# Kernel optimization log

Measured on AMD Instinct MI355X. Metric: run time of the kernel, lower is better.

Reference implementation:

```python
import math
import jax, jax.numpy as jnp
import numpy as np

L, B, E, NDIM = 4096, 4, 1024, 16


def setup_inputs() -> dict:
    key = jax.random.key(0)
    ks = jax.random.split(key, 6)
    x = jax.random.normal(ks[0], (L, B, E), dtype=jnp.float32)
    alpha = jax.random.normal(ks[1], (2 * E, NDIM, 1), dtype=jnp.float32) * 0.2
    delta = jax.random.normal(ks[2], (2 * E, NDIM, 1), dtype=jnp.float32) * 0.2
    # beta init: N(0, 0.02) + alternating +-1 along ndim
    val = np.ones((NDIM, 1), dtype=np.float32)
    val[1::2] = -1.0
    beta = jax.random.normal(ks[3], (2 * E, NDIM, 1), dtype=jnp.float32) * 0.02 + jnp.asarray(val)
    gamma = jax.random.normal(ks[4], (2 * E, NDIM), dtype=jnp.float32)
    omega = jax.random.normal(ks[5], (E,), dtype=jnp.float32)
    return {"x": x, "alpha": alpha, "delta": delta, "beta": beta, "gamma": gamma, "omega": omega}


def reference(x, alpha, delta, beta, gamma, omega):
    seq_len, bsz, embed_dim = x.shape
    ndim = alpha.shape[1]
    scale = math.sqrt(1.0 / ndim)

    residual = x * omega  # (L, B, E)
    xc = jnp.transpose(x, (1, 2, 0))  # (B, E, L)

    a = jax.nn.sigmoid(alpha)
    d = jax.nn.sigmoid(delta)
    q = 1.0 - a * d          # (2E, ndim, 1)
    p = a * beta             # (2E, ndim, 1)

    t = jnp.arange(seq_len, dtype=x.dtype)          # (L,)
    vander = t[None, None, :] * jnp.log(q)          # (2E, ndim, L)
    kernel = p * jnp.exp(vander)                    # (2E, ndim, L)
    k = jnp.einsum('dnl,dn->dl', kernel, gamma * scale)  # (2E, L)

    fft_len = 2 * seq_len  # seq_len + kernel_size (truncation=None)
    k1, k2 = k[:embed_dim], k[embed_dim:]
    # bidirectional + shift: causal part padded right, flipped anti-causal padded left
    kb = jnp.pad(k1, ((0, 0), (0, seq_len))) + jnp.pad(k2[:, ::-1], ((0, 0), (seq_len, 0)))  # (E, 2L)

    k_f = jnp.fft.rfft(kb, n=fft_len)   # (E, L+1) complex
    x_f = jnp.fft.rfft(xc, n=fft_len)   # (B, E, L+1) complex
    out = jnp.fft.irfft(x_f * k_f, n=fft_len)[..., :seq_len]  # (B, E, L)
    out = out.astype(x.dtype)

    return jax.nn.silu(jnp.transpose(out, (2, 0, 1)) + residual)  # (L, B, E)
```

## Files before the change

kernel.cpp:

```cpp
#include <hip/hip_runtime.h>
#include <hip/hip_fp16.h>
#include <math.h>

#define L_  4096
#define B_  4
#define E_  1024
#define ND  16
#define BE  (B_*E_)
#define COLS (BE*ND)

#define OFF_Q   0
#define OFF_W   (2*E_*ND)
#define OFF_QC  (2*2*E_*ND)
#define OFF_FS  (3*2*E_*ND)

__device__ __forceinline__ float sigm(float x){ return 1.0f/(1.0f+__expf(-x)); }

__global__ void k_params(const float* __restrict__ al,
                         const float* __restrict__ de,
                         const float* __restrict__ be,
                         const float* __restrict__ ga,
                         float* __restrict__ ws, int lg){
    int i = blockIdx.x*256 + threadIdx.x;
    float a = sigm(al[i]);
    float d = sigm(de[i]);
    float q = 1.0f - a*d;
    float w = a*be[i]*ga[i]*0.25f;
    float qc = q;
    for(int k=0;k<lg;k++) qc *= qc;
    ws[OFF_Q+i]=q; ws[OFF_W+i]=w; ws[OFF_QC+i]=qc;
}

template<int CK>
__global__ __launch_bounds__(256) void k_summ_t(const float* __restrict__ x,
                                                float* __restrict__ ws){
    const int bid = blockIdx.x;
    const int c  = bid >> 4;
    const int b  = (bid >> 2) & 3;
    const int eg = bid & 3;
    const int e  = eg*256 + threadIdx.x;
    const float* Q = ws + OFF_Q;
    float qf[ND], qb[ND], F[ND], G[ND], pw[ND];
    #pragma unroll
    for(int n=0;n<ND;n++){
        qf[n]=Q[e*ND+n]; qb[n]=Q[(E_+e)*ND+n];
        F[n]=0.f; G[n]=0.f; pw[n]=1.f;
    }
    const float* xp = x + (size_t)(c*CK)*BE + b*E_ + e;
    #pragma unroll 4
    for(int i=0;i<CK;i++){
        float xv = xp[(size_t)i*BE];
        #pragma unroll
        for(int n=0;n<ND;n++){
            F[n]=fmaf(qf[n],F[n],xv);
            G[n]=fmaf(pw[n],xv,G[n]);
            pw[n]*=qb[n];
        }
    }
    const int col = (b*E_+e)*ND;
    float* Fp = ws + OFF_FS + (size_t)c*COLS + col;
    float* Gp = ws + OFF_FS + (size_t)(L_/CK)*COLS + (size_t)c*COLS + col;
    #pragma unroll
    for(int n=0;n<ND;n++){ Fp[n]=F[n]; Gp[n]=G[n]; }
}

template<int CK, int CW>
__global__ __launch_bounds__(256) void k_out2_t(const float* __restrict__ x,
                                                const float* __restrict__ om,
                                                const float* __restrict__ ws,
                                                float* __restrict__ out){
    constexpr int NC = L_/CK;
    __shared__ __half part[CK*256];
    const int tid = threadIdx.x;
    const int bid = blockIdx.x;
    const int c  = bid >> 4;
    const int b  = (bid >> 2) & 3;
    const int eg = bid & 3;
    const int e  = eg*256 + tid;
    const float* Q = ws + OFF_Q;
    const float* W = ws + OFF_W;
    const float omg = om[e];
    const int col = (b*E_+e)*ND;
    const float* xp = x + (size_t)(c*CK)*BE + b*E_ + e;
    const float* FS = ws + OFF_FS;
    const float* GR = ws + OFF_FS + (size_t)NC*COLS;

    {
        float st[ND];
        {
            float pw[ND], qcf[ND];
            #pragma unroll
            for(int n=0;n<ND;n++){ st[n]=0.f; pw[n]=1.f; qcf[n]=ws[OFF_QC+e*ND+n]; }
            int jm = (c < CW) ? c : CW;
            for(int j=1;j<=jm;j++){
                const float4* Fp = (const float4*)(FS + (size_t)(c-j)*COLS + col);
                #pragma unroll
                for(int v=0;v<4;v++){
                    float4 f = Fp[v];
                    st[4*v+0]=fmaf(pw[4*v+0],f.x,st[4*v+0]);
                    st[4*v+1]=fmaf(pw[4*v+1],f.y,st[4*v+1]);
                    st[4*v+2]=fmaf(pw[4*v+2],f.z,st[4*v+2]);
                    st[4*v+3]=fmaf(pw[4*v+3],f.w,st[4*v+3]);
                }
                #pragma unroll
                for(int n=0;n<ND;n++) pw[n]*=qcf[n];
            }
        }
        float q1[ND], w1[ND];
        #pragma unroll
        for(int n=0;n<ND;n++){ q1[n]=Q[e*ND+n]; w1[n]=W[e*ND+n]; }
        #pragma unroll 4
        for(int i=0;i<CK;i++){
            float xv = xp[(size_t)i*BE];
            float acc = xv*omg;
            #pragma unroll
            for(int n=0;n<ND;n++){ st[n]=fmaf(q1[n],st[n],xv); acc=fmaf(w1[n],st[n],acc); }
            part[i*256+tid] = __float2half_rn(acc);
        }
    }

    {
        float rt[ND];
        {
            float pw[ND], qcb[ND];
            #pragma unroll
            for(int n=0;n<ND;n++){ rt[n]=0.f; pw[n]=1.f; qcb[n]=ws[OFF_QC+(E_+e)*ND+n]; }
            int jm = NC-1-c; if(jm > CW) jm = CW;
            for(int j=1;j<=jm;j++){
                const float4* Gp = (const float4*)(GR + (size_t)(c+j)*COLS + col);
                #pragma unroll
                for(int v=0;v<4;v++){
                    float4 g = Gp[v];
                    rt[4*v+0]=fmaf(pw[4*v+0],g.x,rt[4*v+0]);
                    rt[4*v+1]=fmaf(pw[4*v+1],g.y,rt[4*v+1]);
                    rt[4*v+2]=fmaf(pw[4*v+2],g.z,rt[4*v+2]);
                    rt[4*v+3]=fmaf(pw[4*v+3],g.w,rt[4*v+3]);
                }
                #pragma unroll
                for(int n=0;n<ND;n++) pw[n]*=qcb[n];
            }
        }
        float q2[ND], w2[ND];
        #pragma unroll
        for(int n=0;n<ND;n++){ q2[n]=Q[(E_+e)*ND+n]; w2[n]=W[(E_+e)*ND+n]; }
        float* op = out + (size_t)(c*CK)*BE + b*E_ + e;
        #pragma unroll 4
        for(int i=CK-1;i>=0;i--){
            float acc = __half2float(part[i*256+tid]);
            #pragma unroll
            for(int n=0;n<ND;n++) acc = fmaf(w2[n], rt[n], acc);
            float z = acc;
            op[(size_t)i*BE] = z / (1.0f + __expf(-z));
            float xv = xp[(size_t)i*BE];
            #pragma unroll
            for(int n=0;n<ND;n++) rt[n]=fmaf(q2[n],rt[n],xv);
        }
    }
}

extern "C" void kernel_launch(void* const* d_in, const int* in_sizes, int n_in,
                              void* d_out, int out_size, void* d_ws, size_t ws_size,
                              hipStream_t stream) {
    const float* x  = (const float*)d_in[0];
    const float* al = (const float*)d_in[1];
    const float* de = (const float*)d_in[2];
    const float* be = (const float*)d_in[3];
    const float* ga = (const float*)d_in[4];
    const float* om = (const float*)d_in[5];
    float* ws = (float*)d_ws;
    float* out = (float*)d_out;

    size_t need32 = ((size_t)OFF_FS + 2*(size_t)(L_/32)*COLS) * sizeof(float);
    if (ws_size >= need32) {
        k_params<<<dim3((2*E_*ND)/256), dim3(256), 0, stream>>>(al, de, be, ga, ws, 5);
        k_summ_t<32>   <<<dim3((L_/32)*B_*(E_/256)), dim3(256), 0, stream>>>(x, ws);
        k_out2_t<32,4> <<<dim3((L_/32)*B_*(E_/256)), dim3(256), 0, stream>>>(x, om, ws, out);
    } else {
        k_params<<<dim3((2*E_*ND)/256), dim3(256), 0, stream>>>(al, de, be, ga, ws, 6);
        k_summ_t<64>   <<<dim3((L_/64)*B_*(E_/256)), dim3(256), 0, stream>>>(x, ws);
        k_out2_t<64,4> <<<dim3((L_/64)*B_*(E_/256)), dim3(256), 0, stream>>>(x, om, ws, out);
    }
}
```

Measured before the change: 191.7 us.

## Stage x tiles in shared memory with float4 loads, restructure chunk scans

Both chunk kernels now use 128-thread blocks that load the x chunk into a shared-memory tile with coalesced float4 loads. The output kernel writes its results back through the same tile as float4 stores, so the repeated strided per-element global reads of x disappear. The summary kernel computes G with a backward Horner recurrence instead of tracking powers. The carry-in loops fold neighbouring chunk states in Horner order, dropping the separate power updates. Forward partial sums now stay in fp32 registers (acc[CK]) instead of an fp16 shared buffer, which raises register pressure, and the fallback path's window is reduced to CW=2.

New measurement: 373.8 us. 95.0% more time.

```diff
diff --git a/kernel.cpp b/kernel.cpp
--- a/kernel.cpp
+++ b/kernel.cpp
@@ -32,129 +32,160 @@
 }
 
 template<int CK>
-__global__ __launch_bounds__(256) void k_summ_t(const float* __restrict__ x,
+__global__ __launch_bounds__(128) void k_summ_t(const float* __restrict__ x,
                                                 float* __restrict__ ws){
+    constexpr int NC = L_/CK;
+    __shared__ float tile[CK][128];
+    const int tid = threadIdx.x;
     const int bid = blockIdx.x;
-    const int c  = bid >> 4;
-    const int b  = (bid >> 2) & 3;
-    const int eg = bid & 3;
-    const int e  = eg*256 + threadIdx.x;
+    const int c  = bid >> 5;
+    const int b  = (bid >> 3) & 3;
+    const int eg = bid & 7;
+    const int e  = eg*128 + tid;
+    const int t32 = tid & 31, r0 = tid >> 5;
+    {
+        const float* gp = x + (size_t)(c*CK + r0)*BE + b*E_ + eg*128 + 4*t32;
+        #pragma unroll
+        for(int it=0; it<CK/4; ++it)
+            *(float4*)&tile[it*4 + r0][4*t32] = *(const float4*)(gp + (size_t)it*4*BE);
+    }
+    __syncthreads();
     const float* Q = ws + OFF_Q;
-    float qf[ND], qb[ND], F[ND], G[ND], pw[ND];
-    #pragma unroll
-    for(int n=0;n<ND;n++){
-        qf[n]=Q[e*ND+n]; qb[n]=Q[(E_+e)*ND+n];
-        F[n]=0.f; G[n]=0.f; pw[n]=1.f;
-    }
-    const float* xp = x + (size_t)(c*CK)*BE + b*E_ + e;
-    #pragma unroll 4
-    for(int i=0;i<CK;i++){
-        float xv = xp[(size_t)i*BE];
-        #pragma unroll
-        for(int n=0;n<ND;n++){
-            F[n]=fmaf(qf[n],F[n],xv);
-            G[n]=fmaf(pw[n],xv,G[n]);
-            pw[n]*=qb[n];
-        }
-    }
     const int col = (b*E_+e)*ND;
-    float* Fp = ws + OFF_FS + (size_t)c*COLS + col;
-    float* Gp = ws + OFF_FS + (size_t)(L_/CK)*COLS + (size_t)c*COLS + col;
-    #pragma unroll
-    for(int n=0;n<ND;n++){ Fp[n]=F[n]; Gp[n]=G[n]; }
+    {
+        float qf[ND], F[ND];
+        #pragma unroll
+        for(int n=0;n<ND;n++){ qf[n]=Q[e*ND+n]; F[n]=0.f; }
+        #pragma unroll
+        for(int i=0;i<CK;i++){
+            float xv = tile[i][tid];
+            #pragma unroll
+            for(int n=0;n<ND;n++) F[n]=fmaf(qf[n],F[n],xv);
+        }
+        float* Fp = ws + OFF_FS + (size_t)c*COLS + col;
+        #pragma unroll
+        for(int n=0;n<ND;n++) Fp[n]=F[n];
+    }
+    {
+        float qb[ND], G[ND];
+        #pragma unroll
+        for(int n=0;n<ND;n++){ qb[n]=Q[(E_+e)*ND+n]; G[n]=0.f; }
+        #pragma unroll
+        for(int i=CK-1;i>=0;i--){
+            float xv = tile[i][tid];
+            #pragma unroll
+            for(int n=0;n<ND;n++) G[n]=fmaf(qb[n],G[n],xv);
+        }
+        float* Gp = ws + OFF_FS + (size_t)NC*COLS + (size_t)c*COLS + col;
+        #pragma unroll
+        for(int n=0;n<ND;n++) Gp[n]=G[n];
+    }
 }
 
 template<int CK, int CW>
-__global__ __launch_bounds__(256) void k_out2_t(const float* __restrict__ x,
+__global__ __launch_bounds__(128) void k_out2_t(const float* __restrict__ x,
                                                 const float* __restrict__ om,
                                                 const float* __restrict__ ws,
                                                 float* __restrict__ out){
     constexpr int NC = L_/CK;
-    __shared__ __half part[CK*256];
+    __shared__ float tile[CK][128];
     const int tid = threadIdx.x;
     const int bid = blockIdx.x;
-    const int c  = bid >> 4;
-    const int b  = (bid >> 2) & 3;
-    const int eg = bid & 3;
-    const int e  = eg*256 + tid;
-    const float* Q = ws + OFF_Q;
-    const float* W = ws + OFF_W;
+    const int c  = bid >> 5;
+    const int b  = (bid >> 3) & 3;
+    const int eg = bid & 7;
+    const int e  = eg*128 + tid;
+    const int t32 = tid & 31, r0 = tid >> 5;
+    const size_t goff = (size_t)(c*CK + r0)*BE + b*E_ + eg*128 + 4*t32;
+    {
+        const float* gp = x + goff;
+        #pragma unroll
+        for(int it=0; it<CK/4; ++it)
+            *(float4*)&tile[it*4 + r0][4*t32] = *(const float4*)(gp + (size_t)it*4*BE);
+    }
+    __syncthreads();
+    const float* Q  = ws + OFF_Q;
+    const float* W  = ws + OFF_W;
+    const float* FS = ws + OFF_FS;
+    const float* GR = FS + (size_t)NC*COLS;
+    const int col = (b*E_+e)*ND;
     const float omg = om[e];
-    const int col = (b*E_+e)*ND;
-    const float* xp = x + (size_t)(c*CK)*BE + b*E_ + e;
-    const float* FS = ws + OFF_FS;
-    const float* GR = ws + OFF_FS + (size_t)NC*COLS;
+    float acc[CK];
 
     {
         float st[ND];
         {
-            float pw[ND], qcf[ND];
-            #pragma unroll
-            for(int n=0;n<ND;n++){ st[n]=0.f; pw[n]=1.f; qcf[n]=ws[OFF_QC+e*ND+n]; }
+            float qc[ND];
+            #pragma unroll
+            for(int n=0;n<ND;n++){ qc[n]=ws[OFF_QC+e*ND+n]; st[n]=0.f; }
             int jm = (c < CW) ? c : CW;
-            for(int j=1;j<=jm;j++){
+            for(int j=jm; j>=1; --j){
                 const float4* Fp = (const float4*)(FS + (size_t)(c-j)*COLS + col);
                 #pragma unroll
                 for(int v=0;v<4;v++){
                     float4 f = Fp[v];
-                    st[4*v+0]=fmaf(pw[4*v+0],f.x,st[4*v+0]);
-                    st[4*v+1]=fmaf(pw[4*v+1],f.y,st[4*v+1]);
-                    st[4*v+2]=fmaf(pw[4*v+2],f.z,st[4*v+2]);
-                    st[4*v+3]=fmaf(pw[4*v+3],f.w,st[4*v+3]);
+                    st[4*v+0]=fmaf(qc[4*v+0],st[4*v+0],f.x);
+                    st[4*v+1]=fmaf(qc[4*v+1],st[4*v+1],f.y);
+                    st[4*v+2]=fmaf(qc[4*v+2],st[4*v+2],f.z);
+                    st[4*v+3]=fmaf(qc[4*v+3],st[4*v+3],f.w);
                 }
-                #pragma unroll
-                for(int n=0;n<ND;n++) pw[n]*=qcf[n];
             }
         }
         float q1[ND], w1[ND];
         #pragma unroll
         for(int n=0;n<ND;n++){ q1[n]=Q[e*ND+n]; w1[n]=W[e*ND+n]; }
-        #pragma unroll 4
+        #pragma unroll
         for(int i=0;i<CK;i++){
-            float xv = xp[(size_t)i*BE];
-            float acc = xv*omg;
-            #pragma unroll
-            for(int n=0;n<ND;n++){ st[n]=fmaf(q1[n],st[n],xv); acc=fmaf(w1[n],st[n],acc); }
-            part[i*256+tid] = __float2half_rn(acc);
+            float xv = tile[i][tid];
+            #pragma unroll
+            for(int n=0;n<ND;n++) st[n]=fmaf(q1[n],st[n],xv);
+            float a0=xv*omg, a1=0.f;
+            #pragma unroll
+            for(int n=0;n<8;n++){ a0=fmaf(w1[n],st[n],a0); a1=fmaf(w1[n+8],st[n+8],a1); }
+            acc[i]=a0+a1;
         }
     }
 
     {
         float rt[ND];
         {
-            float pw[ND], qcb[ND];
-            #pragma unroll
-            for(int n=0;n<ND;n++){ rt[n]=0.f; pw[n]=1.f; qcb[n]=ws[OFF_QC+(E_+e)*ND+n]; }
-            int jm = NC-1-c; if(jm > CW) jm = CW;
-            for(int j=1;j<=jm;j++){
+            float qc[ND];
+            #pragma unroll
+            for(int n=0;n<ND;n++){ qc[n]=ws[OFF_QC+(E_+e)*ND+n]; rt[n]=0.f; }
+            int jm = NC-1-c; if(jm>CW) jm=CW;
+            for(int j=jm; j>=1; --j){
                 const float4* Gp = (const float4*)(GR + (size_t)(c+j)*COLS + col);
                 #pragma unroll
                 for(int v=0;v<4;v++){
                     float4 g = Gp[v];
-                    rt[4*v+0]=fmaf(pw[4*v+0],g.x,rt[4*v+0]);
-                    rt[4*v+1]=fmaf(pw[4*v+1],g.y,rt[4*v+1]);
-                    rt[4*v+2]=fmaf(pw[4*v+2],g.z,rt[4*v+2]);
-                    rt[4*v+3]=fmaf(pw[4*v+3],g.w,rt[4*v+3]);
+                    rt[4*v+0]=fmaf(qc[4*v+0],rt[4*v+0],g.x);
+                    rt[4*v+1]=fmaf(qc[4*v+1],rt[4*v+1],g.y);
+                    rt[4*v+2]=fmaf(qc[4*v+2],rt[4*v+2],g.z);
+                    rt[4*v+3]=fmaf(qc[4*v+3],rt[4*v+3],g.w);
                 }
-                #pragma unroll
-                for(int n=0;n<ND;n++) pw[n]*=qcb[n];
             }
         }
         float q2[ND], w2[ND];
         #pragma unroll
         for(int n=0;n<ND;n++){ q2[n]=Q[(E_+e)*ND+n]; w2[n]=W[(E_+e)*ND+n]; }
-        float* op = out + (size_t)(c*CK)*BE + b*E_ + e;
-        #pragma unroll 4
+        #pragma unroll
         for(int i=CK-1;i>=0;i--){
-            float acc = __half2float(part[i*256+tid]);
-            #pragma unroll
-            for(int n=0;n<ND;n++) acc = fmaf(w2[n], rt[n], acc);
-            float z = acc;
-            op[(size_t)i*BE] = z / (1.0f + __expf(-z));
-            float xv = xp[(size_t)i*BE];
+            float xv = tile[i][tid];
+            float a0=acc[i], a1=0.f;
+            #pragma unroll
+            for(int n=0;n<8;n++){ a0=fmaf(w2[n],rt[n],a0); a1=fmaf(w2[n+8],rt[n+8],a1); }
+            float z=a0+a1;
+            tile[i][tid] = z / (1.0f + __expf(-z));
             #pragma unroll
             for(int n=0;n<ND;n++) rt[n]=fmaf(q2[n],rt[n],xv);
         }
+    }
+    __syncthreads();
+    {
+        float* op = out + goff;
+        #pragma unroll
+        for(int it=0; it<CK/4; ++it)
+            *(float4*)(op + (size_t)it*4*BE) = *(const float4*)&tile[it*4 + r0][4*t32];
     }
 }
 
@@ -170,14 +201,14 @@
     float* ws = (float*)d_ws;
     float* out = (float*)d_out;
 
-    size_t need32 = ((size_t)OFF_FS + 2*(size_t)(L_/32)*COLS) * sizeof(float);
+    size_t need32 = ((size_t)OFF_FS + 2ull*(L_/32)*COLS) * sizeof(float);
     if (ws_size >= need32) {
         k_params<<<dim3((2*E_*ND)/256), dim3(256), 0, stream>>>(al, de, be, ga, ws, 5);
-        k_summ_t<32>   <<<dim3((L_/32)*B_*(E_/256)), dim3(256), 0, stream>>>(x, ws);
-        k_out2_t<32,4> <<<dim3((L_/32)*B_*(E_/256)), dim3(256), 0, stream>>>(x, om, ws, out);
+        k_summ_t<32>   <<<dim3((L_/32)*32), dim3(128), 0, stream>>>(x, ws);
+        k_out2_t<32,4> <<<dim3((L_/32)*32), dim3(128), 0, stream>>>(x, om, ws, out);
     } else {
         k_params<<<dim3((2*E_*ND)/256), dim3(256), 0, stream>>>(al, de, be, ga, ws, 6);
-        k_summ_t<64>   <<<dim3((L_/64)*B_*(E_/256)), dim3(256), 0, stream>>>(x, ws);
-        k_out2_t<64,4> <<<dim3((L_/64)*B_*(E_/256)), dim3(256), 0, stream>>>(x, om, ws, out);
-    }
-}
+        k_summ_t<64>   <<<dim3((L_/64)*32), dim3(128), 0, stream>>>(x, ws);
+        k_out2_t<64,2> <<<dim3((L_/64)*32), dim3(128), 0, stream>>>(x, om, ws, out);
+    }
+}
```
